# Kernel optimization log

Hardware: AMD Instinct MI355X
Metric: run time of the kernel (lower is better)

The kernel has to match this reference:

```python
import jax, jax.numpy as jnp
import numpy as np

B, S, HID = 4, 1024, 1024
H, HK, D = 16, 8, 64
EPS = 1e-6
THETA = 10000.0
ROPE_SCALE = 1.0


def _rms_norm(x, gamma=None):
    # RMSNorm over head_dim; Gemma-style (1+gamma) scale, v_norm has no scale.
    v = x * jax.lax.rsqrt(jnp.mean(x * x, axis=-1, keepdims=True) + EPS)
    return v if gamma is None else v * (1.0 + gamma)


def _rope_1d(x, pos, theta, scale):
    # x: [B,S,h,d], pos: [B,S] -> rotate-half RoPE along d
    d = x.shape[-1]
    inv_freq = 1.0 / (theta ** (jnp.arange(0, d, 2, dtype=jnp.float32) / d))  # [d/2]
    ang = (pos.astype(jnp.float32) / scale)[..., None] * inv_freq             # [B,S,d/2]
    cos = jnp.cos(ang)[:, :, None, :]
    sin = jnp.sin(ang)[:, :, None, :]
    x1, x2 = x[..., : d // 2], x[..., d // 2 :]
    return jnp.concatenate([x1 * cos - x2 * sin, x2 * cos + x1 * sin], axis=-1)


def _multidim_rope(x, positions_xy, theta, scale):
    # split head_dim in half: first half rotated by x-position, second by y-position
    d = x.shape[-1]
    xh, yh = x[..., : d // 2], x[..., d // 2 :]
    return jnp.concatenate(
        [_rope_1d(xh, positions_xy[..., 0], theta, scale),
         _rope_1d(yh, positions_xy[..., 1], theta, scale)], axis=-1)


def setup_inputs() -> dict:
    key = jax.random.key(0)
    ks = jax.random.split(key, 8)
    std = 0.02
    return {
        "hidden_states": jax.random.normal(ks[0], (B, S, HID), jnp.float32),
        "Wq": jax.random.normal(ks[1], (HID, H * D), jnp.float32) * std,
        "Wk": jax.random.normal(ks[2], (HID, HK * D), jnp.float32) * std,
        "Wv": jax.random.normal(ks[3], (HID, HK * D), jnp.float32) * std,
        "Wo": jax.random.normal(ks[4], (H * D, HID), jnp.float32) * std,
        "q_gamma": jax.random.normal(ks[5], (D,), jnp.float32) * 0.02,
        "k_gamma": jax.random.normal(ks[6], (D,), jnp.float32) * 0.02,
        "positions_xy": jax.random.randint(ks[7], (B, S, 2), 0, 32, dtype=jnp.int32),
        "attention_mask": jnp.ones((B, S, S), dtype=bool),
    }


def reference(hidden_states, Wq, Wk, Wv, Wo, q_gamma, k_gamma, positions_xy, attention_mask):
    b, s, _ = hidden_states.shape
    q = (hidden_states @ Wq).reshape(b, s, H, D)
    k = (hidden_states @ Wk).reshape(b, s, HK, D)
    v = (hidden_states @ Wv).reshape(b, s, HK, D)
    q = _rms_norm(q, q_gamma)
    k = _rms_norm(k, k_gamma)
    v = _rms_norm(v)  # no scale
    q = _multidim_rope(q, positions_xy, THETA, ROPE_SCALE).transpose(0, 2, 1, 3)  # [B,H,S,D]
    k = _multidim_rope(k, positions_xy, THETA, ROPE_SCALE).transpose(0, 2, 1, 3)  # [B,HK,S,D]
    v = v.transpose(0, 2, 1, 3)                                                   # [B,HK,S,D]
    groups = H // HK
    k = jnp.repeat(k, groups, axis=1)  # GQA expand -> [B,H,S,D]
    v = jnp.repeat(v, groups, axis=1)
    # scale=1.0 per the original SDPA call (no 1/sqrt(d))
    logits = jnp.einsum("bhqd,bhkd->bhqk", q, k)
    neg = jnp.asarray(jnp.finfo(logits.dtype).min, logits.dtype)
    logits = jnp.where(attention_mask[:, None, :, :], logits, neg)
    probs = jax.nn.softmax(logits.astype(jnp.float32), axis=-1).astype(q.dtype)
    out = jnp.einsum("bhqk,bhkd->bhqd", probs, v)
    out = out.transpose(0, 2, 1, 3).reshape(b, s, H * D)
    return out @ Wo
```

## Files before the change

### kernel.cpp

```cpp
#include <hip/hip_runtime.h>
#include <hip/hip_bf16.h>
#include <stdint.h>

typedef __attribute__((ext_vector_type(8))) short short8;
typedef __attribute__((ext_vector_type(4))) short s16x4;
typedef __attribute__((ext_vector_type(4))) float f32x4;
typedef __attribute__((ext_vector_type(16))) float f32x16;

#define MFMA16(a, b, c) __builtin_amdgcn_mfma_f32_16x16x32_bf16(a, b, c, 0, 0, 0)
#define MFMA32(a, b, c) __builtin_amdgcn_mfma_f32_32x32x16_bf16(a, b, c, 0, 0, 0)

__device__ __forceinline__ unsigned short f2bf_u(float f) {
  union { float f; uint32_t u; } x; x.f = f;
  uint32_t r = (x.u + 0x7fffu + ((x.u >> 16) & 1u)) >> 16;
  return (unsigned short)r;
}
__device__ __forceinline__ short f2bf(float f) { return (short)f2bf_u(f); }

__device__ __forceinline__ uint32_t pack_bf2(float lo, float hi) {
  __hip_bfloat162 h = __float22bfloat162_rn(make_float2(lo, hi));
  union { __hip_bfloat162 h; uint32_t u; } c; c.h = h;
  return c.u;
}

__device__ __forceinline__ void gload_lds16(const void* g, void* lds) {
  __builtin_amdgcn_global_load_lds(
      (const __attribute__((address_space(1))) uint32_t*)(uintptr_t)g,
      (__attribute__((address_space(3))) uint32_t*)(uintptr_t)lds,
      16, 0, 0);
}

__global__ __launch_bounds__(256) void convert_bf16_kernel(
    const float* __restrict__ in, short* __restrict__ out, int n4) {
  int i = blockIdx.x * 256 + threadIdx.x;
  if (i >= n4) return;
  float4 v = reinterpret_cast<const float4*>(in)[i];
  short4 o;
  o.x = f2bf(v.x); o.y = f2bf(v.y); o.z = f2bf(v.z); o.w = f2bf(v.w);
  reinterpret_cast<short4*>(out)[i] = o;
}

__global__ __launch_bounds__(256) void transpose_all_kernel(
    const float* __restrict__ Wq, const float* __restrict__ Wk,
    const float* __restrict__ Wv, const float* __restrict__ Wo,
    short* __restrict__ WTQKV, short* __restrict__ WOT) {
  __shared__ float tile[32][33];
  int yb = blockIdx.y;
  const float* src; short* dst; int N; int yy;
  if (yb < 32)      { src = Wq; dst = WTQKV;                       N = 1024; yy = yb; }
  else if (yb < 48) { src = Wk; dst = WTQKV + (size_t)1024 * 1024; N = 512;  yy = yb - 32; }
  else if (yb < 64) { src = Wv; dst = WTQKV + (size_t)1536 * 1024; N = 512;  yy = yb - 48; }
  else              { src = Wo; dst = WOT;                         N = 1024; yy = yb - 64; }
  int k0 = blockIdx.x * 32, n0 = yy * 32;
  int tx = threadIdx.x, ty = threadIdx.y;
#pragma unroll
  for (int i = 0; i < 4; ++i)
    tile[ty + 8 * i][tx] = src[(size_t)(k0 + ty + 8 * i) * N + n0 + tx];
  __syncthreads();
#pragma unroll
  for (int i = 0; i < 4; ++i)
    dst[(size_t)(n0 + ty + 8 * i) * 1024 + k0 + tx] = f2bf(tile[tx][ty + 8 * i]);
}

__global__ __launch_bounds__(256) void gemm_qkv_fused(
    const short* __restrict__ A, const short* __restrict__ BT,
    const float* __restrict__ qg, const float* __restrict__ kg,
    const int* __restrict__ pos,
    short* __restrict__ Qp, short* __restrict__ Kp, short* __restrict__ Vt) {
  const int K = 1024;
  __shared__ short As[2 * 128 * 32];
  __shared__ short Bs[2 * 128 * 32];
  int wg = blockIdx.x + gridDim.x * blockIdx.y;
  int lid = (wg & 7) * 64 + (wg >> 3);
  int m0 = (lid & 31) * 128, n0 = (lid >> 5) * 128;
  int t = threadIdx.x;
  int w = t >> 6, lane = t & 63;
  int wr = w >> 1, wc = w & 1;
  int lr = lane & 15, lg = lane >> 4;

  f32x4 acc[4][4] = {};

  for (int k0 = 0; k0 < K; k0 += 64) {
    __syncthreads();
#pragma unroll
    for (int i = 0; i < 4; ++i) {
      int q = t + 256 * i;
      int kk = q >> 9, row = (q >> 2) & 127, c = q & 3;
      gload_lds16(A + (size_t)(m0 + row) * K + k0 + kk * 32 + c * 8, &As[q * 8]);
      gload_lds16(BT + (size_t)(n0 + row) * K + k0 + kk * 32 + c * 8, &Bs[q * 8]);
    }
    __syncthreads();
#pragma unroll
    for (int kk = 0; kk < 2; ++kk) {
      short8 af[4], bf[4];
#pragma unroll
      for (int mi = 0; mi < 4; ++mi)
        af[mi] = *(const short8*)&As[kk * 4096 + (wr * 64 + mi * 16 + lr) * 32 + lg * 8];
#pragma unroll
      for (int ni = 0; ni < 4; ++ni)
        bf[ni] = *(const short8*)&Bs[kk * 4096 + (wc * 64 + ni * 16 + lr) * 32 + lg * 8];
      __builtin_amdgcn_s_setprio(1);
#pragma unroll
      for (int mi = 0; mi < 4; ++mi)
#pragma unroll
        for (int ni = 0; ni < 4; ++ni)
          acc[mi][ni] = MFMA16(af[mi], bf[ni], acc[mi][ni]);
      __builtin_amdgcn_s_setprio(0);
    }
  }

  int g = (n0 >> 6) + wc;
  int row0 = m0 + wr * 64;
  const int2* posv = (const int2*)pos;

  if (g < 24) {
    const float* gsrc = (g < 16) ? qg : kg;
    short* dst = (g < 16) ? Qp : Kp;
    int nh = (g < 16) ? 16 : 8;
    int h = (g < 16) ? g : g - 16;
    float gscale = (g < 16) ? 1.4426950408889634f : 1.0f;
    float gam[4];
#pragma unroll
    for (int ni = 0; ni < 4; ++ni) gam[ni] = (1.0f + gsrc[ni * 16 + lr]) * gscale;
    float invf = exp2f((float)lr * -0.8304820237218405f);
#pragma unroll
    for (int mi = 0; mi < 4; ++mi) {
      f32x4 ss = acc[mi][0] * acc[mi][0];
#pragma unroll
      for (int ni = 1; ni < 4; ++ni) ss += acc[mi][ni] * acc[mi][ni];
#pragma unroll
      for (int m2 = 1; m2 < 16; m2 <<= 1)
#pragma unroll
        for (int r = 0; r < 4; ++r) ss[r] += __shfl_xor(ss[r], m2);
#pragma unroll
      for (int r = 0; r < 4; ++r) {
        int row = row0 + mi * 16 + lg * 4 + r;
        float inv = rsqrtf(ss[r] * 0.015625f + 1e-6f);
        float v0 = acc[mi][0][r] * inv * gam[0];
        float v1 = acc[mi][1][r] * inv * gam[1];
        float v2 = acc[mi][2][r] * inv * gam[2];
        float v3 = acc[mi][3][r] * inv * gam[3];
        int2 pp = posv[row];
        float sx, cx, sy, cy;
        __sincosf((float)pp.x * invf, &sx, &cx);
        __sincosf((float)pp.y * invf, &sy, &cy);
        float o0 = v0 * cx - v1 * sx, o1 = v1 * cx + v0 * sx;
        float o2 = v2 * cy - v3 * sy, o3 = v3 * cy + v2 * sy;
        int s = row & 1023, bb = row >> 10;
        short* base = dst + ((size_t)((bb * nh + h) * 1024 + s)) * 64;
        base[lr]      = f2bf(o0);
        base[lr + 16] = f2bf(o1);
        base[lr + 32] = f2bf(o2);
        base[lr + 48] = f2bf(o3);
      }
    }
  } else {
    int hk = g - 24;
#pragma unroll
    for (int mi = 0; mi < 4; ++mi) {
      f32x4 ss = acc[mi][0] * acc[mi][0];
#pragma unroll
      for (int ni = 1; ni < 4; ++ni) ss += acc[mi][ni] * acc[mi][ni];
#pragma unroll
      for (int m2 = 1; m2 < 16; m2 <<= 1)
#pragma unroll
        for (int r = 0; r < 4; ++r) ss[r] += __shfl_xor(ss[r], m2);
      f32x4 inv;
#pragma unroll
      for (int r = 0; r < 4; ++r) inv[r] = rsqrtf(ss[r] * 0.015625f + 1e-6f);
      int row = row0 + mi * 16 + lg * 4;
      int s0 = row & 1023, bb = row >> 10;
#pragma unroll
      for (int ni = 0; ni < 4; ++ni) {
        short4 sv;
        sv.x = f2bf(acc[mi][ni][0] * inv[0]);
        sv.y = f2bf(acc[mi][ni][1] * inv[1]);
        sv.z = f2bf(acc[mi][ni][2] * inv[2]);
        sv.w = f2bf(acc[mi][ni][3] * inv[3]);
        int d = ni * 16 + lr;
        *(short4*)&Vt[((size_t)((bb * 8 + hk) * 64 + d)) * 1024 + s0] = sv;
      }
    }
  }
}

__global__ __launch_bounds__(256) void gemm_bf16_bn64(
    const short* __restrict__ A, const short* __restrict__ BT,
    float* __restrict__ C, int M, int N, int K) {
  __shared__ short As[2 * 128 * 32];
  __shared__ short Bs[2 * 64 * 32];
  int wg = blockIdx.x + gridDim.x * blockIdx.y;
  int lid = (wg & 7) * 64 + (wg >> 3);
  int m0 = (lid & 31) * 128, n0 = (lid >> 5) * 64;
  int t = threadIdx.x;
  int w = t >> 6, lane = t & 63;
  int lr = lane & 15, lg = lane >> 4;

  f32x4 acc[2][4] = {};

  for (int k0 = 0; k0 < K; k0 += 64) {
    __syncthreads();
#pragma unroll
    for (int i = 0; i < 4; ++i) {
      int q = t + 256 * i;
      int kk = q >> 9, row = (q >> 2) & 127, c = q & 3;
      gload_lds16(A + (size_t)(m0 + row) * K + k0 + kk * 32 + c * 8, &As[q * 8]);
    }
#pragma unroll
    for (int i = 0; i < 2; ++i) {
      int q = t + 256 * i;
      int kk = q >> 8, row = (q >> 2) & 63, c = q & 3;
      gload_lds16(BT + (size_t)(n0 + row) * K + k0 + kk * 32 + c * 8, &Bs[q * 8]);
    }
    __syncthreads();
#pragma unroll
    for (int kk = 0; kk < 2; ++kk) {
      short8 af[2], bf[4];
#pragma unroll
      for (int mi = 0; mi < 2; ++mi)
        af[mi] = *(const short8*)&As[kk * 4096 + (w * 32 + mi * 16 + lr) * 32 + lg * 8];
#pragma unroll
      for (int ni = 0; ni < 4; ++ni)
        bf[ni] = *(const short8*)&Bs[kk * 2048 + (ni * 16 + lr) * 32 + lg * 8];
      __builtin_amdgcn_s_setprio(1);
#pragma unroll
      for (int mi = 0; mi < 2; ++mi)
#pragma unroll
        for (int ni = 0; ni < 4; ++ni)
          acc[mi][ni] = MFMA16(af[mi], bf[ni], acc[mi][ni]);
      __builtin_amdgcn_s_setprio(0);
    }
  }
#pragma unroll
  for (int mi = 0; mi < 2; ++mi)
#pragma unroll
    for (int ni = 0; ni < 4; ++ni) {
      int row = m0 + w * 32 + mi * 16 + lg * 4;
      int col = n0 + ni * 16 + lr;
#pragma unroll
      for (int r = 0; r < 4; ++r)
        C[(size_t)(row + r) * N + col] = acc[mi][ni][r];
    }
}

__global__ __launch_bounds__(256) void attn_kernel(
    const short* __restrict__ Qp, const short* __restrict__ Kp,
    const short* __restrict__ Vt, short* __restrict__ attn) {
  __shared__ short Ks[2][4096];
  __shared__ short Vs[2][4096];
  int wg = blockIdx.x;
  int xcd = wg & 7, slot = wg >> 3;
  int group = xcd * 8 + (slot >> 3);
  int qblk = slot & 7;
  int b = group >> 4, h = group & 15;
  int hk = h >> 1;
  int t = threadIdx.x;
  int w = t >> 6, lane = t & 63;
  int l31 = lane & 31, hh = lane >> 5;
  int xr = l31 & 7;
  int q0 = qblk * 128 + w * 32;

  const short* Qb = Qp + ((size_t)(b * 16 + h) * 1024) * 64;
  const short* Kb = Kp + ((size_t)(b * 8 + hk) * 1024) * 64;
  const short* Vb = Vt + ((size_t)(b * 8 + hk) * 64) * 1024;

  short8 qf[4];
#pragma unroll
  for (int dk = 0; dk < 4; ++dk)
    qf[dk] = *(const short8*)&Qb[(q0 + l31) * 64 + dk * 16 + hh * 8];

  f32x16 acc[2] = {};
  f32x4 lsumv = {};

  auto STAGE = [&](short* ksb, short* vsb, int kt) {
    int kv0 = kt * 64;
#pragma unroll
    for (int i = 0; i < 2; ++i) {
      int q = t + 256 * i;
      int kv = q >> 3, cd = q & 7, cs = cd ^ (kv & 7);
      gload_lds16(Kb + (size_t)(kv0 + kv) * 64 + cs * 8, &ksb[q * 8]);
    }
#pragma unroll
    for (int i = 0; i < 2; ++i) {
      int q = t + 256 * i;
      int d = q >> 3, cd = q & 7, cs = cd ^ (d & 7);
      gload_lds16(Vb + (size_t)d * 1024 + kv0 + cs * 8, &vsb[q * 8]);
    }
  };

  auto COMPUTE = [&](const short* ksb, const short* vsb) {
#pragma unroll
    for (int kvb2 = 0; kvb2 < 2; ++kvb2) {
      f32x16 sv = {};
      __builtin_amdgcn_s_setprio(1);
#pragma unroll
      for (int dk = 0; dk < 4; ++dk) {
        short8 kf = *(const short8*)&ksb[(kvb2 * 32 + l31) * 64 + ((dk * 2 + hh) ^ xr) * 8];
        sv = MFMA32(kf, qf[dk], sv);
      }
      __builtin_amdgcn_s_setprio(0);
      float p[16];
#pragma unroll
      for (int r = 0; r < 16; ++r) p[r] = exp2f(sv[r]);
#pragma unroll
      for (int r = 0; r < 16; r += 4) {
        lsumv[0] += p[r]; lsumv[1] += p[r + 1];
        lsumv[2] += p[r + 2]; lsumv[3] += p[r + 3];
      }
      uint32_t pk8[8];
#pragma unroll
      for (int j = 0; j < 8; ++j) pk8[j] = pack_bf2(p[2 * j], p[2 * j + 1]);
#pragma unroll
      for (int kvc = 0; kvc < 2; ++kvc) {
        union { uint32_t u[4]; short8 s; } pb;
#pragma unroll
        for (int j = 0; j < 4; ++j) pb.u[j] = pk8[kvc * 4 + j];
        int cg = kvb2 * 4 + kvc * 2;
        __builtin_amdgcn_s_setprio(1);
#pragma unroll
        for (int db2 = 0; db2 < 2; ++db2) {
          int dd = db2 * 32 + l31;
          union { s16x4 h4[2]; short8 s; } vu;
          vu.h4[0] = *(const s16x4*)&vsb[dd * 64 + ((cg ^ xr) * 8) + 4 * hh];
          vu.h4[1] = *(const s16x4*)&vsb[dd * 64 + (((cg + 1) ^ xr) * 8) + 4 * hh];
          acc[db2] = MFMA32(vu.s, pb.s, acc[db2]);
        }
        __builtin_amdgcn_s_setprio(0);
      }
    }
  };

  STAGE(Ks[0], Vs[0], 0);
  __syncthreads();
  int cur = 0;
  for (int kt = 0; kt < 15; ++kt) {
    STAGE(Ks[cur ^ 1], Vs[cur ^ 1], kt + 1);
    __builtin_amdgcn_sched_barrier(0);
    COMPUTE(Ks[cur], Vs[cur]);
    __syncthreads();
    cur ^= 1;
  }
  COMPUTE(Ks[cur], Vs[cur]);

  float lsum = (lsumv[0] + lsumv[1]) + (lsumv[2] + lsumv[3]);
  lsum += __shfl_xor(lsum, 32);
  float inv = 1.0f / lsum;
  short* orow = attn + ((size_t)(b * 1024 + q0 + l31)) * 1024 + h * 64;
#pragma unroll
  for (int db2 = 0; db2 < 2; ++db2)
#pragma unroll
    for (int g2 = 0; g2 < 4; ++g2) {
      int d0 = db2 * 32 + g2 * 8 + 4 * hh;
      uint32_t w0 = pack_bf2(acc[db2][g2 * 4 + 0] * inv, acc[db2][g2 * 4 + 1] * inv);
      uint32_t w1 = pack_bf2(acc[db2][g2 * 4 + 2] * inv, acc[db2][g2 * 4 + 3] * inv);
      *(uint2*)&orow[d0] = make_uint2(w0, w1);
    }
}

extern "C" void kernel_launch(void* const* d_in, const int* in_sizes, int n_in,
                              void* d_out, int out_size, void* d_ws, size_t ws_size,
                              hipStream_t stream) {
  const float* X  = (const float*)d_in[0];
  const float* Wq = (const float*)d_in[1];
  const float* Wk = (const float*)d_in[2];
  const float* Wv = (const float*)d_in[3];
  const float* Wo = (const float*)d_in[4];
  const float* qg = (const float*)d_in[5];
  const float* kg = (const float*)d_in[6];
  const int* pos  = (const int*)d_in[7];
  float* out = (float*)d_out;

  char* ws = (char*)d_ws;
  short* XB    = (short*)(ws);
  short* WTQKV = (short*)(ws + ((size_t)8 << 20));
  short* WOT   = (short*)(ws + ((size_t)12 << 20));
  short* QP    = (short*)(ws + ((size_t)14 << 20));
  short* KP    = (short*)(ws + ((size_t)22 << 20));
  short* VT    = (short*)(ws + ((size_t)26 << 20));
  short* ATT   = (short*)(ws + ((size_t)30 << 20));

  convert_bf16_kernel<<<4096, 256, 0, stream>>>(X, XB, 1048576);
  transpose_all_kernel<<<dim3(32, 96), dim3(32, 8), 0, stream>>>(Wq, Wk, Wv, Wo, WTQKV, WOT);

  gemm_qkv_fused<<<dim3(32, 16), 256, 0, stream>>>(XB, WTQKV, qg, kg, pos, QP, KP, VT);
  attn_kernel<<<512, 256, 0, stream>>>(QP, KP, VT, ATT);
  gemm_bf16_bn64<<<dim3(32, 16), 256, 0, stream>>>(ATT, WOT, out, 4096, 1024, 1024);
}
```

Measured before the change: 100.8 us.

## Split attention into 128-thread blocks, permute V layout, and use finer sync

Attention blocks shrink from 256 threads (128 queries) to 128 threads (64 queries), and the grid doubles to 1024 blocks for more parallelism and occupancy. The V-transpose writer in the QKV GEMM permutes the sequence index so the PV MFMA operand can be read as a single 16-byte LDS load instead of two 8-byte loads. K and V fragments are preloaded into registers ahead of the MFMAs. __syncthreads is replaced by explicit vmcnt waits and barriers to overlap the next tile's loads. In exchange, each K/V tile is staged from global memory by twice as many blocks, and correctness depends on the permuted layout and vmcnt count matching exactly.

```diff
diff --git a/kernel.cpp b/kernel.cpp
--- a/kernel.cpp
+++ b/kernel.cpp
@@ -3,7 +3,6 @@
 #include <stdint.h>
 
 typedef __attribute__((ext_vector_type(8))) short short8;
-typedef __attribute__((ext_vector_type(4))) short s16x4;
 typedef __attribute__((ext_vector_type(4))) float f32x4;
 typedef __attribute__((ext_vector_type(16))) float f32x16;
 
@@ -170,6 +169,8 @@
       for (int r = 0; r < 4; ++r) inv[r] = rsqrtf(ss[r] * 0.015625f + 1e-6f);
       int row = row0 + mi * 16 + lg * 4;
       int s0 = row & 1023, bb = row >> 10;
+      int kv = s0 & 63, c = kv >> 3, hb = (kv >> 2) & 1;
+      int sp = (s0 & ~63) | (((c & 6) | hb) << 3) | ((c & 1) << 2);
 #pragma unroll
       for (int ni = 0; ni < 4; ++ni) {
         short4 sv;
@@ -178,7 +179,7 @@
         sv.z = f2bf(acc[mi][ni][2] * inv[2]);
         sv.w = f2bf(acc[mi][ni][3] * inv[3]);
         int d = ni * 16 + lr;
-        *(short4*)&Vt[((size_t)((bb * 8 + hk) * 64 + d)) * 1024 + s0] = sv;
+        *(short4*)&Vt[((size_t)((bb * 8 + hk) * 64 + d)) * 1024 + sp] = sv;
       }
     }
   }
@@ -243,22 +244,22 @@
     }
 }
 
-__global__ __launch_bounds__(256) void attn_kernel(
+__global__ __launch_bounds__(128, 2) void attn_kernel(
     const short* __restrict__ Qp, const short* __restrict__ Kp,
     const short* __restrict__ Vt, short* __restrict__ attn) {
   __shared__ short Ks[2][4096];
   __shared__ short Vs[2][4096];
   int wg = blockIdx.x;
   int xcd = wg & 7, slot = wg >> 3;
-  int group = xcd * 8 + (slot >> 3);
-  int qblk = slot & 7;
+  int group = xcd * 8 + (slot >> 4);
+  int qblk = slot & 15;
   int b = group >> 4, h = group & 15;
   int hk = h >> 1;
   int t = threadIdx.x;
   int w = t >> 6, lane = t & 63;
   int l31 = lane & 31, hh = lane >> 5;
   int xr = l31 & 7;
-  int q0 = qblk * 128 + w * 32;
+  int q0 = qblk * 64 + w * 32;
 
   const short* Qb = Qp + ((size_t)(b * 16 + h) * 1024) * 64;
   const short* Kb = Kp + ((size_t)(b * 8 + hk) * 1024) * 64;
@@ -275,30 +276,38 @@
   auto STAGE = [&](short* ksb, short* vsb, int kt) {
     int kv0 = kt * 64;
 #pragma unroll
-    for (int i = 0; i < 2; ++i) {
-      int q = t + 256 * i;
+    for (int i = 0; i < 4; ++i) {
+      int q = t + 128 * i;
       int kv = q >> 3, cd = q & 7, cs = cd ^ (kv & 7);
       gload_lds16(Kb + (size_t)(kv0 + kv) * 64 + cs * 8, &ksb[q * 8]);
     }
 #pragma unroll
-    for (int i = 0; i < 2; ++i) {
-      int q = t + 256 * i;
-      int d = q >> 3, cd = q & 7, cs = cd ^ (d & 7);
-      gload_lds16(Vb + (size_t)d * 1024 + kv0 + cs * 8, &vsb[q * 8]);
+    for (int i = 0; i < 4; ++i) {
+      int q = t + 128 * i;
+      int d = q >> 3, bi = q & 7, bs = bi ^ (d & 7);
+      gload_lds16(Vb + (size_t)d * 1024 + kv0 + bs * 8, &vsb[q * 8]);
     }
   };
 
   auto COMPUTE = [&](const short* ksb, const short* vsb) {
 #pragma unroll
     for (int kvb2 = 0; kvb2 < 2; ++kvb2) {
+      short8 kf[4];
+#pragma unroll
+      for (int dk = 0; dk < 4; ++dk)
+        kf[dk] = *(const short8*)&ksb[(kvb2 * 32 + l31) * 64 + ((dk * 2 + hh) ^ xr) * 8];
       f32x16 sv = {};
       __builtin_amdgcn_s_setprio(1);
 #pragma unroll
-      for (int dk = 0; dk < 4; ++dk) {
-        short8 kf = *(const short8*)&ksb[(kvb2 * 32 + l31) * 64 + ((dk * 2 + hh) ^ xr) * 8];
-        sv = MFMA32(kf, qf[dk], sv);
-      }
+      for (int dk = 0; dk < 4; ++dk) sv = MFMA32(kf[dk], qf[dk], sv);
       __builtin_amdgcn_s_setprio(0);
+      short8 vf[4];
+#pragma unroll
+      for (int kvc = 0; kvc < 2; ++kvc)
+#pragma unroll
+        for (int db2 = 0; db2 < 2; ++db2)
+          vf[kvc * 2 + db2] = *(const short8*)
+              &vsb[(db2 * 32 + l31) * 64 + (((kvb2 * 4 + kvc * 2 + hh) ^ xr)) * 8];
       float p[16];
 #pragma unroll
       for (int r = 0; r < 16; ++r) p[r] = exp2f(sv[r]);
@@ -315,31 +324,29 @@
         union { uint32_t u[4]; short8 s; } pb;
 #pragma unroll
         for (int j = 0; j < 4; ++j) pb.u[j] = pk8[kvc * 4 + j];
-        int cg = kvb2 * 4 + kvc * 2;
         __builtin_amdgcn_s_setprio(1);
 #pragma unroll
-        for (int db2 = 0; db2 < 2; ++db2) {
-          int dd = db2 * 32 + l31;
-          union { s16x4 h4[2]; short8 s; } vu;
-          vu.h4[0] = *(const s16x4*)&vsb[dd * 64 + ((cg ^ xr) * 8) + 4 * hh];
-          vu.h4[1] = *(const s16x4*)&vsb[dd * 64 + (((cg + 1) ^ xr) * 8) + 4 * hh];
-          acc[db2] = MFMA32(vu.s, pb.s, acc[db2]);
-        }
+        for (int db2 = 0; db2 < 2; ++db2)
+          acc[db2] = MFMA32(vf[kvc * 2 + db2], pb.s, acc[db2]);
         __builtin_amdgcn_s_setprio(0);
       }
     }
   };
 
   STAGE(Ks[0], Vs[0], 0);
-  __syncthreads();
   int cur = 0;
   for (int kt = 0; kt < 15; ++kt) {
     STAGE(Ks[cur ^ 1], Vs[cur ^ 1], kt + 1);
+    asm volatile("s_waitcnt vmcnt(8)" ::: "memory");
+    __builtin_amdgcn_s_barrier();
     __builtin_amdgcn_sched_barrier(0);
     COMPUTE(Ks[cur], Vs[cur]);
-    __syncthreads();
+    __builtin_amdgcn_sched_barrier(0);
+    __builtin_amdgcn_s_barrier();
     cur ^= 1;
   }
+  asm volatile("s_waitcnt vmcnt(0)" ::: "memory");
+  __builtin_amdgcn_s_barrier();
   COMPUTE(Ks[cur], Vs[cur]);
 
   float lsum = (lsumv[0] + lsumv[1]) + (lsumv[2] + lsumv[3]);
@@ -383,6 +390,6 @@
   transpose_all_kernel<<<dim3(32, 96), dim3(32, 8), 0, stream>>>(Wq, Wk, Wv, Wo, WTQKV, WOT);
 
   gemm_qkv_fused<<<dim3(32, 16), 256, 0, stream>>>(XB, WTQKV, qg, kg, pos, QP, KP, VT);
-  attn_kernel<<<512, 256, 0, stream>>>(QP, KP, VT, ATT);
+  attn_kernel<<<1024, 128, 0, stream>>>(QP, KP, VT, ATT);
   gemm_bf16_bn64<<<dim3(32, 16), 256, 0, stream>>>(ATT, WOT, out, 4096, 1024, 1024);
 }
```

Measured after the change: 99.30 us. Within noise of the previous version (-1.5%).
